# Kernel tuning notes

Hardware: AMD Instinct MI355X
Metric: run time of the kernel (lower is better)

## Reference

```python
import jax, jax.numpy as jnp
import numpy as np
from jax import lax

T, V, E = 8, 10000, 100000
C_IN, H, DS, C_OUT = 128, 256, 16, 64


def setup_inputs() -> dict:
    key = jax.random.key(0)
    ks = jax.random.split(key, 32)
    def nrm(k, shp, s=0.02):
        return jax.random.normal(k, shp, jnp.float32) * s
    inp = {}
    inp['xs'] = jax.random.normal(ks[0], (T, V, C_IN), jnp.float32)
    inp['edge_index'] = jax.random.randint(ks[1], (T, 2, E), 0, V, jnp.int64)
    # pre token mixer: depthwise conv1d over time, kernel 3, pad 1
    inp['w_pre'] = nrm(ks[2], (C_IN, 3), 0.3)
    inp['b_pre'] = jnp.zeros((C_IN,), jnp.float32)
    # per-layer params; layer 0 input C_IN, layer 1 input H
    for i, f in enumerate([C_IN, H]):
        o = 3 + i * 9
        inp[f'w_res{i}'] = nrm(ks[o + 0], (f, H))
        inp[f'b_res{i}'] = jnp.zeros((H,), jnp.float32)
        inp[f'w_self{i}'] = nrm(ks[o + 1], (f, H))
        inp[f'w_neigh{i}'] = nrm(ks[o + 2], (f, H))
        inp[f'b_sage{i}'] = jnp.zeros((H,), jnp.float32)
        inp[f'a_log{i}'] = nrm(ks[o + 3], (H, DS), 0.5)  # Lambda = exp(-exp(a_log)) in (0,1)
        inp[f'B{i}'] = nrm(ks[o + 4], (H, DS), 0.1)
        inp[f'w_mix{i}'] = nrm(ks[o + 5], (H * DS, H))
        inp[f'b_mix{i}'] = jnp.zeros((H,), jnp.float32)
    inp['w_out'] = nrm(ks[25], (H, C_OUT))
    inp['b_out'] = jnp.zeros((C_OUT,), jnp.float32)
    return inp


def _token_mix(xs, w, b):
    # xs: [T, V, C]; depthwise conv over time, kernel 3, zero pad 1
    xp = jnp.pad(xs, ((1, 1), (0, 0), (0, 0)))
    return xp[0:T] * w[:, 0] + xp[1:T + 1] * w[:, 1] + xp[2:T + 2] * w[:, 2] + b


def _sage(x, ei, w_self, w_neigh, b):
    # x: [V, C]; ei: [2, E]; mean aggregation of source features at target nodes
    src, dst = ei[0], ei[1]
    agg = jax.ops.segment_sum(x[src], dst, num_segments=V)          # [V, C]
    deg = jax.ops.segment_sum(jnp.ones((E,), x.dtype), dst, num_segments=V)
    mean = agg / jnp.maximum(deg, 1.0)[:, None]
    return x @ w_self + mean @ w_neigh + b


def _layer(xs, ei, w_res, b_res, w_self, w_neigh, b_sage, a_log, Bp, w_mix, b_mix):
    xsr = xs @ w_res + b_res                                        # [T, V, H]
    h = jax.vmap(_sage, in_axes=(0, 0, None, None, None))(xs, ei, w_self, w_neigh, b_sage)
    lam = jnp.exp(-jnp.exp(a_log))                                  # [H, DS]
    def step(state, x_t):
        state = lam * state + x_t[:, :, None] * Bp                  # [V, H, DS]
        y = jax.nn.relu(state.reshape(V, H * DS)) @ w_mix + b_mix   # [V, H]
        return state, y
    _, ys = lax.scan(step, jnp.zeros((V, H, DS), xs.dtype), h)
    return ys + xsr


def reference(xs, edge_index, w_pre, b_pre,
              w_res0, b_res0, w_self0, w_neigh0, b_sage0, a_log0, B0, w_mix0, b_mix0,
              w_res1, b_res1, w_self1, w_neigh1, b_sage1, a_log1, B1, w_mix1, b_mix1,
              w_out, b_out):
    xs = _token_mix(xs, w_pre, b_pre)
    xs = _layer(xs, edge_index, w_res0, b_res0, w_self0, w_neigh0, b_sage0, a_log0, B0, w_mix0, b_mix0)
    xs = _layer(xs, edge_index, w_res1, b_res1, w_self1, w_neigh1, b_sage1, a_log1, B1, w_mix1, b_mix1)
    return xs[-1] @ w_out + b_out
```

## Files before the change

### kernel.cpp

```cpp
#include <hip/hip_runtime.h>
#include <cstdint>
#include <cstddef>

#define T_DIM 8
#define V_DIM 10000
#define E_DIM 100000
#define M_ALL (T_DIM * V_DIM)

typedef __attribute__((ext_vector_type(8))) short short8;
typedef __attribute__((ext_vector_type(4))) float floatx4;

__device__ __forceinline__ unsigned int f2bf(float f) {
    union { float f; unsigned int u; } v; v.f = f;
    unsigned int u = v.u;
    u = u + 0x7FFFu + ((u >> 16) & 1u);
    return u >> 16;
}
__device__ __forceinline__ float bf2f(unsigned int s) {
    union { unsigned int u; float f; } v; v.u = s << 16;
    return v.f;
}
__device__ __forceinline__ short8 relu8(short8 x) {
    const short8 z = {0,0,0,0,0,0,0,0};
    return __builtin_elementwise_max(x, z);
}
union PK { uint4 u; short8 s; };

__global__ void pack_b_kernel(const float* __restrict__ w, unsigned short* __restrict__ out,
                              int K, int Nw, int NTN_tot, int nt_off, int kt_off) {
    int tid = blockIdx.x * blockDim.x + threadIdx.x;
    int total = (K >> 5) * (Nw >> 4) * 64;
    if (tid >= total) return;
    int lane = tid & 63;
    int f = tid >> 6;
    int ntn_w = Nw >> 4;
    int nt = f % ntn_w;
    int kt = f / ntn_w;
    int kbase = kt * 32 + ((lane >> 4) << 3);
    int n = nt * 16 + (lane & 15);
    unsigned int vals[8];
#pragma unroll
    for (int j = 0; j < 8; ++j)
        vals[j] = f2bf(w[(size_t)(kbase + j) * Nw + n]);
    uint4 pk;
    pk.x = vals[0] | (vals[1] << 16);
    pk.y = vals[2] | (vals[3] << 16);
    pk.z = vals[4] | (vals[5] << 16);
    pk.w = vals[6] | (vals[7] << 16);
    size_t fo = (size_t)(kt + kt_off) * NTN_tot + nt_off + nt;
    *(uint4*)(out + (fo * 64 + lane) * 8) = pk;
}

__global__ void token_mix_kernel(const float* __restrict__ xs, const float* __restrict__ w_pre,
                                 const float* __restrict__ b_pre, unsigned short* __restrict__ ob) {
    const int S = V_DIM * 128;
    int tid = blockIdx.x * blockDim.x + threadIdx.x;
    if (tid >= T_DIM * S / 4) return;
    int e = tid * 4;
    int t = e / S;
    int c = e & 127;
    floatx4 xm = {0.f,0.f,0.f,0.f}, xp = {0.f,0.f,0.f,0.f};
    floatx4 x0 = *(const floatx4*)(xs + e);
    if (t > 0)          xm = *(const floatx4*)(xs + e - S);
    if (t < T_DIM - 1)  xp = *(const floatx4*)(xs + e + S);
    uint2 p; unsigned int b[4];
#pragma unroll
    for (int j = 0; j < 4; ++j) {
        int cc = c + j;
        float r = xm[j]*w_pre[cc*3+0] + x0[j]*w_pre[cc*3+1] + xp[j]*w_pre[cc*3+2] + b_pre[cc];
        b[j] = f2bf(r);
    }
    p.x = b[0] | (b[1] << 16);
    p.y = b[2] | (b[3] << 16);
    *(uint2*)(ob + e) = p;
}

__global__ void lam_kernel(const float* __restrict__ a0, const float* __restrict__ a1,
                           float* __restrict__ lam0, float* __restrict__ lam1) {
    int i = blockIdx.x * blockDim.x + threadIdx.x;
    if (i >= 4096) return;
    lam0[i] = expf(-expf(a0[i]));
    lam1[i] = expf(-expf(a1[i]));
}

__global__ void bias_prep_kernel(const float* __restrict__ bs0, const float* __restrict__ bs1,
                                 const float* __restrict__ bm0, const float* __restrict__ br0,
                                 const float* __restrict__ bm1, const float* __restrict__ br1,
                                 float* __restrict__ bcat0, float* __restrict__ bcat1,
                                 float* __restrict__ bmt0, float* __restrict__ bmt1) {
    int i = blockIdx.x * blockDim.x + threadIdx.x;
    if (i < 512) {
        bcat0[i] = (i < 256) ? bs0[i] : 0.f;
        bcat1[i] = (i < 256) ? bs1[i] : 0.f;
    }
    if (i < 256) {
        bmt0[i] = bm0[i] + br0[i];
        bmt1[i] = bm1[i] + br1[i];
    }
}

__global__ void deg_kernel(const int* __restrict__ ei, int* __restrict__ deg_cnt) {
    int tid = blockIdx.x * blockDim.x + threadIdx.x;
    if (tid >= T_DIM * E_DIM) return;
    int t = tid / E_DIM;
    int e = tid - t * E_DIM;
    int dst = ei[(size_t)t * 2 * E_DIM + E_DIM + e];
    if ((unsigned)dst < V_DIM) atomicAdd(deg_cnt + t * V_DIM + dst, 1);
}

__global__ void invdeg_kernel(const int* __restrict__ deg_cnt, float* __restrict__ inv) {
    int tid = blockIdx.x * blockDim.x + threadIdx.x;
    if (tid >= T_DIM * V_DIM) return;
    inv[tid] = 1.0f / (float)max(deg_cnt[tid], 1);
}

__global__ __launch_bounds__(1024)
void scan_kernel(const int* __restrict__ deg_cnt, int* __restrict__ rowptr) {
    __shared__ int sums[1024];
    int t = blockIdx.x;
    const int* d = deg_cnt + t * V_DIM;
    int* rp = rowptr + t * (V_DIM + 1);
    int tid = threadIdx.x;
    int base = tid * 10;
    int loc[10]; int s = 0;
#pragma unroll
    for (int j = 0; j < 10; ++j) {
        int v = base + j;
        int x = (v < V_DIM) ? d[v] : 0;
        loc[j] = s; s += x;
    }
    sums[tid] = s;
    __syncthreads();
    for (int o = 1; o < 1024; o <<= 1) {
        int v = (tid >= o) ? sums[tid - o] : 0;
        __syncthreads();
        sums[tid] += v;
        __syncthreads();
    }
    int prev = (tid == 0) ? 0 : sums[tid - 1];
#pragma unroll
    for (int j = 0; j < 10; ++j) {
        int v = base + j;
        if (v < V_DIM) rp[v] = prev + loc[j];
    }
    if (tid == 1023) rp[V_DIM] = sums[1023];
}

__global__ void fill_kernel(const int* __restrict__ ei, const int* __restrict__ rowptr,
                            int* __restrict__ fill_cnt, int* __restrict__ srcs) {
    int tid = blockIdx.x * blockDim.x + threadIdx.x;
    if (tid >= T_DIM * E_DIM) return;
    int t = tid / E_DIM;
    int e = tid - t * E_DIM;
    const int* eit = ei + (size_t)t * 2 * E_DIM;
    int src = eit[e];
    int dst = eit[E_DIM + e];
    if ((unsigned)src >= V_DIM || (unsigned)dst >= V_DIM) return;
    int pos = rowptr[t * (V_DIM + 1) + dst] + atomicAdd(fill_cnt + t * V_DIM + dst, 1);
    srcs[(size_t)t * E_DIM + pos] = src;
}

__global__ void gather_pack_kernel(const unsigned short* __restrict__ xn, const int* __restrict__ srcs,
                                   const int* __restrict__ rowptr, const float* __restrict__ invdeg,
                                   const unsigned short* __restrict__ hb,
                                   unsigned short* __restrict__ hpack) {
    int gw = (blockIdx.x * blockDim.x + threadIdx.x) >> 6;
    int lane = threadIdx.x & 63;
    if (gw >= T_DIM * V_DIM) return;
    int t = gw / V_DIM;
    int v = gw - t * V_DIM;
    const int* rp = rowptr + t * (V_DIM + 1);
    int beg = rp[v], end = rp[v + 1];
    const int* st = srcs + (size_t)t * E_DIM;
    const unsigned short* xnt = xn + (size_t)t * V_DIM * 256;
    float a0 = 0.f, a1 = 0.f, a2 = 0.f, a3 = 0.f;
    for (int i = beg; i < end; ++i) {
        int s = st[i];
        uint2 p = *(const uint2*)(xnt + (size_t)s * 256 + lane * 4);
        a0 += bf2f(p.x & 0xffffu);
        a1 += bf2f(p.x >> 16);
        a2 += bf2f(p.y & 0xffffu);
        a3 += bf2f(p.y >> 16);
    }
    float inv = invdeg[t * V_DIM + v];
    uint2 h = *(const uint2*)(hb + ((size_t)t * V_DIM + v) * 256 + lane * 4);
    a0 = a0 * inv + bf2f(h.x & 0xffffu);
    a1 = a1 * inv + bf2f(h.x >> 16);
    a2 = a2 * inv + bf2f(h.y & 0xffffu);
    a3 = a3 * inv + bf2f(h.y >> 16);
    unsigned short* op = hpack + (size_t)v * 2048 + (size_t)(lane * 4) * 8 + t;
    op[0]  = (unsigned short)f2bf(a0);
    op[8]  = (unsigned short)f2bf(a1);
    op[16] = (unsigned short)f2bf(a2);
    op[24] = (unsigned short)f2bf(a3);
}

template<int KT>
__global__ __launch_bounds__(256, 4)
void gemm_cat2_kernel(const unsigned short* __restrict__ A, const unsigned short* __restrict__ Bp,
                      const float* __restrict__ bias, unsigned short* __restrict__ d_self,
                      unsigned short* __restrict__ d_xn, int M) {
    const int w = threadIdx.x >> 6, lane = threadIdx.x & 63;
    const int quad = lane >> 4, l16 = lane & 15;
    const int region = blockIdx.x;
    const int m0 = blockIdx.y * 64;
    constexpr int K = KT * 32;
    floatx4 acc[4][4];
#pragma unroll
    for (int a = 0; a < 4; ++a)
#pragma unroll
        for (int b = 0; b < 4; ++b) acc[a][b] = (floatx4){0.f,0.f,0.f,0.f};
    const unsigned short* arow[4];
#pragma unroll
    for (int mi = 0; mi < 4; ++mi) {
        int r = m0 + mi * 16 + l16;
        if (r > M - 1) r = M - 1;
        arow[mi] = A + (size_t)r * K + quad * 8;
    }
    const unsigned short* bptr = Bp + ((size_t)(region * 16 + w * 4) * 64 + lane) * 8;
#pragma unroll
    for (int kt = 0; kt < KT; ++kt) {
        short8 bfr[4];
#pragma unroll
        for (int i = 0; i < 4; ++i) bfr[i] = *(const short8*)(bptr + i * 512);
        short8 af[4];
#pragma unroll
        for (int mi = 0; mi < 4; ++mi) af[mi] = *(const short8*)(arow[mi]);
#pragma unroll
        for (int mi = 0; mi < 4; ++mi)
#pragma unroll
            for (int i = 0; i < 4; ++i)
                acc[mi][i] = __builtin_amdgcn_mfma_f32_16x16x32_bf16(af[mi], bfr[i], acc[mi][i], 0, 0, 0);
        bptr += 32 * 512;
#pragma unroll
        for (int mi = 0; mi < 4; ++mi) arow[mi] += 32;
    }
#pragma unroll
    for (int mi = 0; mi < 4; ++mi) {
        int rbase = m0 + mi * 16 + quad * 4;
#pragma unroll
        for (int i = 0; i < 4; ++i) {
            int lcol = w * 64 + i * 16 + l16;
            float b = bias[region * 256 + lcol];
#pragma unroll
            for (int rr = 0; rr < 4; ++rr) {
                int row = rbase + rr;
                if (row < M) {
                    float v = acc[mi][i][rr] + b;
                    size_t off = (size_t)row * 256 + lcol;
                    if (region == 0) d_self[off] = (unsigned short)f2bf(v);
                    else             d_xn[off]  = (unsigned short)f2bf(v);
                }
            }
        }
    }
}

template<int NT, int KRT>
__global__ __launch_bounds__(256, 2)
void gemm_mix_rec2_kernel(const unsigned short* __restrict__ hp,
                          const unsigned short* __restrict__ Bp,
                          const unsigned short* __restrict__ Ares,
                          const float* __restrict__ lam,
                          const float* __restrict__ Bv,
                          const float* __restrict__ bias,
                          unsigned short* __restrict__ out) {
    constexpr int KR = KRT * 32;
    __shared__ __align__(16) unsigned short Afrag[2][4 * NT * 64 * 8];
    const int tid = threadIdx.x;
    const int w = tid >> 6, lane = tid & 63;
    const int quad = lane >> 4, l16 = lane & 15;
    const int m0 = blockIdx.x * 16;
    const int prow = tid & 15;
    const int oct  = tid >> 4;
    const int kt_w = oct >> 2, qo = oct & 3;
    const int vr = m0 + prow;

    floatx4 acc[NT][4];
#pragma unroll
    for (int t = 0; t < NT; ++t)
#pragma unroll
        for (int i = 0; i < 4; ++i) acc[t][i] = (floatx4){0.f,0.f,0.f,0.f};

    const unsigned short* bptr = Bp + ((size_t)(w * 4) * 64 + lane) * 8;

    auto compute = [&](int ph, int buf) {
        const int kg = ph * 128 + kt_w * 32 + qo * 8;
        const int ch = kg >> 4;
        PK h8; h8.u = *(const uint4*)(hp + (size_t)vr * 2048 + (size_t)ch * 8);
        floatx4 l0 = *(const floatx4*)(lam + kg);
        floatx4 l1 = *(const floatx4*)(lam + kg + 4);
        floatx4 b0 = *(const floatx4*)(Bv + kg);
        floatx4 b1 = *(const floatx4*)(Bv + kg + 4);
        float s0=0.f,s1=0.f,s2=0.f,s3=0.f,s4=0.f,s5=0.f,s6=0.f,s7=0.f;
        unsigned short* ap = Afrag[buf] + ((size_t)(kt_w * NT) * 64 + qo * 16 + prow) * 8;
#pragma unroll
        for (int t = 0; t < 8; ++t) {
            float hv = bf2f((unsigned int)(unsigned short)h8.s[t]);
            s0 = l0[0]*s0 + hv*b0[0];
            s1 = l0[1]*s1 + hv*b0[1];
            s2 = l0[2]*s2 + hv*b0[2];
            s3 = l0[3]*s3 + hv*b0[3];
            s4 = l1[0]*s4 + hv*b1[0];
            s5 = l1[1]*s5 + hv*b1[1];
            s6 = l1[2]*s6 + hv*b1[2];
            s7 = l1[3]*s7 + hv*b1[3];
            if (NT == 8 || t == 7) {
                PK cv;
                cv.u.x = f2bf(s0) | (f2bf(s1) << 16);
                cv.u.y = f2bf(s2) | (f2bf(s3) << 16);
                cv.u.z = f2bf(s4) | (f2bf(s5) << 16);
                cv.u.w = f2bf(s6) | (f2bf(s7) << 16);
                PK st; st.s = relu8(cv.s);
                *(uint4*)(ap + (size_t)((NT == 8) ? t : 0) * 512) = st.u;
            }
        }
    };
    auto consume = [&](int buf) {
#pragma unroll
        for (int kt = 0; kt < 4; ++kt) {
            short8 bfr[4];
#pragma unroll
            for (int i = 0; i < 4; ++i) bfr[i] = *(const short8*)(bptr + i * 512);
#pragma unroll
            for (int t = 0; t < NT; ++t) {
                short8 af = *(const short8*)(Afrag[buf] + (size_t)((kt * NT + t) * 64 + lane) * 8);
#pragma unroll
                for (int i = 0; i < 4; ++i)
                    acc[t][i] = __builtin_amdgcn_mfma_f32_16x16x32_bf16(af, bfr[i], acc[t][i], 0, 0, 0);
            }
            bptr += 16 * 512;
        }
    };

    compute(0, 0);
    __syncthreads();
    for (int ph = 0; ph < 32; ++ph) {
        if (ph < 31) compute(ph + 1, (ph + 1) & 1);
        consume(ph & 1);
        __syncthreads();
    }

#pragma unroll
    for (int ktr = 0; ktr < KRT; ++ktr) {
        short8 bfr[4];
#pragma unroll
        for (int i = 0; i < 4; ++i) bfr[i] = *(const short8*)(bptr + i * 512);
#pragma unroll
        for (int t = 0; t < NT; ++t) {
            const unsigned short* ar = Ares + ((size_t)t * V_DIM + (size_t)(m0 + l16)) * KR + ktr * 32 + quad * 8;
            short8 af = *(const short8*)ar;
#pragma unroll
            for (int i = 0; i < 4; ++i)
                acc[t][i] = __builtin_amdgcn_mfma_f32_16x16x32_bf16(af, bfr[i], acc[t][i], 0, 0, 0);
        }
        bptr += 16 * 512;
    }
#pragma unroll
    for (int t = 0; t < NT; ++t) {
#pragma unroll
        for (int i = 0; i < 4; ++i) {
            int col = w * 64 + i * 16 + l16;
            float b = bias[col];
#pragma unroll
            for (int rr = 0; rr < 4; ++rr) {
                int row = m0 + quad * 4 + rr;
                out[((size_t)t * V_DIM + row) * 256 + col] = (unsigned short)f2bf(acc[t][i][rr] + b);
            }
        }
    }
}

template<int NT, int NTN_TOT, bool RELU>
__global__ __launch_bounds__(512)
void gemm16_kernel(const unsigned short* __restrict__ A, const unsigned short* __restrict__ Bp,
                   const float* __restrict__ bias, float* __restrict__ outF, int M, int K) {
    const int w = threadIdx.x >> 6, lane = threadIdx.x & 63;
    const int quad = lane >> 4, l16 = lane & 15;
    const int rowgrp = w >> 2, nchunk = w & 3;
    const int m0 = blockIdx.x * 32 + rowgrp * 16;
    const int ntb = nchunk * NT;
    constexpr int Ntot = NTN_TOT * 16;
    floatx4 acc[NT];
#pragma unroll
    for (int i = 0; i < NT; ++i) acc[i] = (floatx4){0.f,0.f,0.f,0.f};
    int r = m0 + l16; if (r > M - 1) r = M - 1;
    const unsigned short* arow = A + (size_t)r * K + quad * 8;
    const int ksteps = K >> 5;
    for (int kt = 0; kt < ksteps; ++kt) {
        short8 af = *(const short8*)(arow + kt * 32);
        if (RELU) af = relu8(af);
#pragma unroll
        for (int i = 0; i < NT; ++i) {
            short8 bf = *(const short8*)(Bp + ((size_t)(kt * NTN_TOT + ntb + i) * 64 + lane) * 8);
            acc[i] = __builtin_amdgcn_mfma_f32_16x16x32_bf16(af, bf, acc[i], 0, 0, 0);
        }
    }
    const int rbase = m0 + quad * 4;
#pragma unroll
    for (int i = 0; i < NT; ++i) {
        int col = (ntb + i) * 16 + l16;
        float b = bias[col];
#pragma unroll
        for (int rr = 0; rr < 4; ++rr) {
            int row = rbase + rr;
            if (row < M)
                outF[(size_t)row * Ntot + col] = acc[i][rr] + b;
        }
    }
}

extern "C" void kernel_launch(void* const* d_in, const int* in_sizes, int n_in,
                              void* d_out, int out_size, void* d_ws, size_t ws_size,
                              hipStream_t stream) {
    const float* xs      = (const float*)d_in[0];
    const int*   ei      = (const int*)d_in[1];
    const float* w_pre   = (const float*)d_in[2];
    const float* b_pre   = (const float*)d_in[3];
    const float* w_res0  = (const float*)d_in[4];
    const float* b_res0  = (const float*)d_in[5];
    const float* w_self0 = (const float*)d_in[6];
    const float* w_neigh0= (const float*)d_in[7];
    const float* b_sage0 = (const float*)d_in[8];
    const float* a_log0  = (const float*)d_in[9];
    const float* B0      = (const float*)d_in[10];
    const float* w_mix0  = (const float*)d_in[11];
    const float* b_mix0  = (const float*)d_in[12];
    const float* w_res1  = (const float*)d_in[13];
    const float* b_res1  = (const float*)d_in[14];
    const float* w_self1 = (const float*)d_in[15];
    const float* w_neigh1= (const float*)d_in[16];
    const float* b_sage1 = (const float*)d_in[17];
    const float* a_log1  = (const float*)d_in[18];
    const float* B1      = (const float*)d_in[19];
    const float* w_mix1  = (const float*)d_in[20];
    const float* b_mix1  = (const float*)d_in[21];
    const float* w_out   = (const float*)d_in[22];
    const float* b_out   = (const float*)d_in[23];

    char* wsB = (char*)d_ws;
    size_t off = 0;
    auto alloc = [&](size_t bytes) {
        char* p = wsB + off;
        off += (bytes + 255) & ~(size_t)255;
        return p;
    };
    unsigned short* x0b   = (unsigned short*)alloc((size_t)M_ALL * 128 * 2);
    unsigned short* hA    = (unsigned short*)alloc((size_t)M_ALL * 256 * 2);
    unsigned short* hB    = (unsigned short*)alloc((size_t)M_ALL * 256 * 2);
    unsigned short* hpack = (unsigned short*)alloc((size_t)V_DIM * 2048 * 2);
    unsigned short* x1b   = (unsigned short*)alloc((size_t)M_ALL * 256 * 2);
    unsigned short* out1_b= (unsigned short*)alloc((size_t)V_DIM * 256 * 2);
    int*            deg_cnt = (int*)alloc((size_t)T_DIM * V_DIM * 4);
    float*          invdeg  = (float*)alloc((size_t)T_DIM * V_DIM * 4);
    int*            rowptr  = (int*)alloc((size_t)T_DIM * (V_DIM + 1) * 4);
    int*            fill_cnt= (int*)alloc((size_t)T_DIM * V_DIM * 4);
    int*            srcs    = (int*)alloc((size_t)T_DIM * E_DIM * 4);
    float*          lam0  = (float*)alloc(4096 * 4);
    float*          lam1  = (float*)alloc(4096 * 4);
    float*          bcat0 = (float*)alloc(512 * 4);
    float*          bcat1 = (float*)alloc(512 * 4);
    float*          bmt0  = (float*)alloc(256 * 4);
    float*          bmt1  = (float*)alloc(256 * 4);
    unsigned short* wcat0p= (unsigned short*)alloc((size_t)128 * 512 * 2);
    unsigned short* wcat1p= (unsigned short*)alloc((size_t)256 * 512 * 2);
    unsigned short* wmix0p= (unsigned short*)alloc((size_t)(4096 + 128) * 256 * 2);
    unsigned short* wmix1p= (unsigned short*)alloc((size_t)(4096 + 256) * 256 * 2);
    unsigned short* woutp = (unsigned short*)alloc((size_t)256 * 64 * 2);
    if (off > ws_size) return;

    auto cdiv = [](int a, int b) { return (a + b - 1) / b; };
    const int gMall = cdiv(M_ALL, 64);
    const int gGat  = cdiv(M_ALL * 64, 256);

    lam_kernel<<<16, 256, 0, stream>>>(a_log0, a_log1, lam0, lam1);
    bias_prep_kernel<<<2, 256, 0, stream>>>(b_sage0, b_sage1, b_mix0, b_res0, b_mix1, b_res1,
                                            bcat0, bcat1, bmt0, bmt1);
    pack_b_kernel<<<cdiv(4*16*64, 256), 256, 0, stream>>>(w_self0,  wcat0p, 128, 256, 32, 0, 0);
    pack_b_kernel<<<cdiv(4*16*64, 256), 256, 0, stream>>>(w_neigh0, wcat0p, 128, 256, 32, 16, 0);
    pack_b_kernel<<<cdiv(8*16*64, 256), 256, 0, stream>>>(w_self1,  wcat1p, 256, 256, 32, 0, 0);
    pack_b_kernel<<<cdiv(8*16*64, 256), 256, 0, stream>>>(w_neigh1, wcat1p, 256, 256, 32, 16, 0);
    pack_b_kernel<<<cdiv(128*16*64, 256), 256, 0, stream>>>(w_mix0, wmix0p, 4096, 256, 16, 0, 0);
    pack_b_kernel<<<cdiv(4*16*64, 256),   256, 0, stream>>>(w_res0, wmix0p, 128,  256, 16, 0, 128);
    pack_b_kernel<<<cdiv(128*16*64, 256), 256, 0, stream>>>(w_mix1, wmix1p, 4096, 256, 16, 0, 0);
    pack_b_kernel<<<cdiv(8*16*64, 256),   256, 0, stream>>>(w_res1, wmix1p, 256,  256, 16, 0, 128);
    pack_b_kernel<<<cdiv(8*4*64, 256), 256, 0, stream>>>(w_out, woutp, 256, 64, 4, 0, 0);

    token_mix_kernel<<<cdiv(T_DIM*V_DIM*128/4, 256), 256, 0, stream>>>(xs, w_pre, b_pre, x0b);
    hipMemsetAsync(deg_cnt, 0, (size_t)T_DIM * V_DIM * 4, stream);
    hipMemsetAsync(fill_cnt, 0, (size_t)T_DIM * V_DIM * 4, stream);
    deg_kernel<<<cdiv(T_DIM*E_DIM, 256), 256, 0, stream>>>(ei, deg_cnt);
    scan_kernel<<<T_DIM, 1024, 0, stream>>>(deg_cnt, rowptr);
    invdeg_kernel<<<cdiv(T_DIM*V_DIM, 256), 256, 0, stream>>>(deg_cnt, invdeg);
    fill_kernel<<<cdiv(T_DIM*E_DIM, 256), 256, 0, stream>>>(ei, rowptr, fill_cnt, srcs);

    gemm_cat2_kernel<4><<<dim3(2, gMall), 256, 0, stream>>>(x0b, wcat0p, bcat0, hA, hB, M_ALL);
    gather_pack_kernel<<<gGat, 256, 0, stream>>>(hB, srcs, rowptr, invdeg, hA, hpack);
    gemm_mix_rec2_kernel<8, 4><<<V_DIM / 16, 256, 0, stream>>>(
        hpack, wmix0p, x0b, lam0, B0, bmt0, x1b);

    gemm_cat2_kernel<8><<<dim3(2, gMall), 256, 0, stream>>>(x1b, wcat1p, bcat1, hA, hB, M_ALL);
    gather_pack_kernel<<<gGat, 256, 0, stream>>>(hB, srcs, rowptr, invdeg, hA, hpack);
    gemm_mix_rec2_kernel<1, 8><<<V_DIM / 16, 256, 0, stream>>>(
        hpack, wmix1p, x1b + (size_t)(T_DIM - 1) * V_DIM * 256, lam1, B1, bmt1, out1_b);

    gemm16_kernel<1, 4, false><<<cdiv(V_DIM,32), 512, 0, stream>>>(
        out1_b, woutp, b_out, (float*)d_out, V_DIM, 256);
}
```

Baseline: 982.9 us.

## Halve mix-kernel phase size, split state work per thread, use hardware bf16 pack

Measured after the change: 997.1 us. Within noise of the previous version (+1.4%).

```diff
diff --git a/kernel.cpp b/kernel.cpp
--- a/kernel.cpp
+++ b/kernel.cpp
@@ -8,6 +8,7 @@
 #define M_ALL (T_DIM * V_DIM)
 
 typedef __attribute__((ext_vector_type(8))) short short8;
+typedef __attribute__((ext_vector_type(4))) short sx4;
 typedef __attribute__((ext_vector_type(4))) float floatx4;
 
 __device__ __forceinline__ unsigned int f2bf(float f) {
@@ -24,7 +25,17 @@
     const short8 z = {0,0,0,0,0,0,0,0};
     return __builtin_elementwise_max(x, z);
 }
+__device__ __forceinline__ sx4 relu4(sx4 x) {
+    const sx4 z = {0,0,0,0};
+    return __builtin_elementwise_max(x, z);
+}
+__device__ __forceinline__ unsigned int cvtpk_bf16(float lo, float hi) {
+    unsigned int r;
+    asm("v_cvt_pk_bf16_f32 %0, %1, %2" : "=v"(r) : "v"(lo), "v"(hi));
+    return r;
+}
 union PK { uint4 u; short8 s; };
+union PK2 { uint2 u; sx4 s; };
 
 __global__ void pack_b_kernel(const float* __restrict__ w, unsigned short* __restrict__ out,
                               int K, int Nw, int NTN_tot, int nt_off, int kt_off) {
@@ -258,7 +269,7 @@
 
 template<int NT, int KRT>
 __global__ __launch_bounds__(256, 2)
-void gemm_mix_rec2_kernel(const unsigned short* __restrict__ hp,
+void gemm_mix_rec3_kernel(const unsigned short* __restrict__ hp,
                           const unsigned short* __restrict__ Bp,
                           const unsigned short* __restrict__ Ares,
                           const float* __restrict__ lam,
@@ -266,14 +277,17 @@
                           const float* __restrict__ bias,
                           unsigned short* __restrict__ out) {
     constexpr int KR = KRT * 32;
-    __shared__ __align__(16) unsigned short Afrag[2][4 * NT * 64 * 8];
+    __shared__ __align__(16) unsigned short Afrag[2][2 * NT * 64 * 8];
     const int tid = threadIdx.x;
     const int w = tid >> 6, lane = tid & 63;
     const int quad = lane >> 4, l16 = lane & 15;
     const int m0 = blockIdx.x * 16;
     const int prow = tid & 15;
-    const int oct  = tid >> 4;
-    const int kt_w = oct >> 2, qo = oct & 3;
+    const int g    = tid >> 4;
+    const int kt_w = g >> 3;
+    const int sub  = g & 7;
+    const int qo   = sub >> 1;
+    const int hf   = sub & 1;
     const int vr = m0 + prow;
 
     floatx4 acc[NT][4];
@@ -285,43 +299,36 @@
     const unsigned short* bptr = Bp + ((size_t)(w * 4) * 64 + lane) * 8;
 
     auto compute = [&](int ph, int buf) {
-        const int kg = ph * 128 + kt_w * 32 + qo * 8;
+        const int kg = ph * 64 + kt_w * 32 + qo * 8 + hf * 4;
         const int ch = kg >> 4;
         PK h8; h8.u = *(const uint4*)(hp + (size_t)vr * 2048 + (size_t)ch * 8);
-        floatx4 l0 = *(const floatx4*)(lam + kg);
-        floatx4 l1 = *(const floatx4*)(lam + kg + 4);
-        floatx4 b0 = *(const floatx4*)(Bv + kg);
-        floatx4 b1 = *(const floatx4*)(Bv + kg + 4);
-        float s0=0.f,s1=0.f,s2=0.f,s3=0.f,s4=0.f,s5=0.f,s6=0.f,s7=0.f;
-        unsigned short* ap = Afrag[buf] + ((size_t)(kt_w * NT) * 64 + qo * 16 + prow) * 8;
+        floatx4 l = *(const floatx4*)(lam + kg);
+        floatx4 b = *(const floatx4*)(Bv + kg);
+        float s0 = 0.f, s1 = 0.f, s2 = 0.f, s3 = 0.f;
+        unsigned short* ap = Afrag[buf] + ((size_t)(kt_w * NT) * 64 + qo * 16 + prow) * 8 + hf * 4;
 #pragma unroll
         for (int t = 0; t < 8; ++t) {
             float hv = bf2f((unsigned int)(unsigned short)h8.s[t]);
-            s0 = l0[0]*s0 + hv*b0[0];
-            s1 = l0[1]*s1 + hv*b0[1];
-            s2 = l0[2]*s2 + hv*b0[2];
-            s3 = l0[3]*s3 + hv*b0[3];
-            s4 = l1[0]*s4 + hv*b1[0];
-            s5 = l1[1]*s5 + hv*b1[1];
-            s6 = l1[2]*s6 + hv*b1[2];
-            s7 = l1[3]*s7 + hv*b1[3];
+            s0 = l[0]*s0 + hv*b[0];
+            s1 = l[1]*s1 + hv*b[1];
+            s2 = l[2]*s2 + hv*b[2];
+            s3 = l[3]*s3 + hv*b[3];
             if (NT == 8 || t == 7) {
-                PK cv;
-                cv.u.x = f2bf(s0) | (f2bf(s1) << 16);
-                cv.u.y = f2bf(s2) | (f2bf(s3) << 16);
-                cv.u.z = f2bf(s4) | (f2bf(s5) << 16);
-                cv.u.w = f2bf(s6) | (f2bf(s7) << 16);
-                PK st; st.s = relu8(cv.s);
-                *(uint4*)(ap + (size_t)((NT == 8) ? t : 0) * 512) = st.u;
+                PK2 cv;
+                cv.u.x = cvtpk_bf16(s0, s1);
+                cv.u.y = cvtpk_bf16(s2, s3);
+                PK2 st; st.s = relu4(cv.s);
+                *(uint2*)(ap + (size_t)((NT == 8) ? t : 0) * 512) = st.u;
             }
         }
     };
     auto consume = [&](int buf) {
 #pragma unroll
-        for (int kt = 0; kt < 4; ++kt) {
+        for (int kt = 0; kt < 2; ++kt) {
             short8 bfr[4];
 #pragma unroll
             for (int i = 0; i < 4; ++i) bfr[i] = *(const short8*)(bptr + i * 512);
+            __builtin_amdgcn_s_setprio(1);
 #pragma unroll
             for (int t = 0; t < NT; ++t) {
                 short8 af = *(const short8*)(Afrag[buf] + (size_t)((kt * NT + t) * 64 + lane) * 8);
@@ -329,14 +336,15 @@
                 for (int i = 0; i < 4; ++i)
                     acc[t][i] = __builtin_amdgcn_mfma_f32_16x16x32_bf16(af, bfr[i], acc[t][i], 0, 0, 0);
             }
+            __builtin_amdgcn_s_setprio(0);
             bptr += 16 * 512;
         }
     };
 
     compute(0, 0);
     __syncthreads();
-    for (int ph = 0; ph < 32; ++ph) {
-        if (ph < 31) compute(ph + 1, (ph + 1) & 1);
+    for (int ph = 0; ph < 64; ++ph) {
+        if (ph < 63) compute(ph + 1, (ph + 1) & 1);
         consume(ph & 1);
         __syncthreads();
     }
@@ -496,12 +504,12 @@
 
     gemm_cat2_kernel<4><<<dim3(2, gMall), 256, 0, stream>>>(x0b, wcat0p, bcat0, hA, hB, M_ALL);
     gather_pack_kernel<<<gGat, 256, 0, stream>>>(hB, srcs, rowptr, invdeg, hA, hpack);
-    gemm_mix_rec2_kernel<8, 4><<<V_DIM / 16, 256, 0, stream>>>(
+    gemm_mix_rec3_kernel<8, 4><<<V_DIM / 16, 256, 0, stream>>>(
         hpack, wmix0p, x0b, lam0, B0, bmt0, x1b);
 
     gemm_cat2_kernel<8><<<dim3(2, gMall), 256, 0, stream>>>(x1b, wcat1p, bcat1, hA, hB, M_ALL);
     gather_pack_kernel<<<gGat, 256, 0, stream>>>(hB, srcs, rowptr, invdeg, hA, hpack);
-    gemm_mix_rec2_kernel<1, 8><<<V_DIM / 16, 256, 0, stream>>>(
+    gemm_mix_rec3_kernel<1, 8><<<V_DIM / 16, 256, 0, stream>>>(
         hpack, wmix1p, x1b + (size_t)(T_DIM - 1) * V_DIM * 256, lam1, B1, bmt1, out1_b);
 
     gemm16_kernel<1, 4, false><<<cdiv(V_DIM,32), 512, 0, stream>>>(
```

## Split mix-recurrence GEMM over time chunks and use hardware bf16 pack

Applied to the files above, without the earlier changes.

Measured after the change: 926.2 us. -5.8%, faster.

```diff
diff --git a/kernel.cpp b/kernel.cpp
--- a/kernel.cpp
+++ b/kernel.cpp
@@ -23,6 +23,11 @@
 __device__ __forceinline__ short8 relu8(short8 x) {
     const short8 z = {0,0,0,0,0,0,0,0};
     return __builtin_elementwise_max(x, z);
+}
+__device__ __forceinline__ unsigned int cvtpk_bf16(float lo, float hi) {
+    unsigned int r;
+    asm("v_cvt_pk_bf16_f32 %0, %1, %2" : "=v"(r) : "v"(lo), "v"(hi));
+    return r;
 }
 union PK { uint4 u; short8 s; };
 
@@ -256,29 +261,31 @@
     }
 }
 
-template<int NT, int KRT>
-__global__ __launch_bounds__(256, 2)
-void gemm_mix_rec2_kernel(const unsigned short* __restrict__ hp,
+template<int NTC, int KRT>
+__global__ __launch_bounds__(256, 3)
+void gemm_mix_rec4_kernel(const unsigned short* __restrict__ hp,
                           const unsigned short* __restrict__ Bp,
                           const unsigned short* __restrict__ Ares,
                           const float* __restrict__ lam,
                           const float* __restrict__ Bv,
                           const float* __restrict__ bias,
-                          unsigned short* __restrict__ out) {
+                          unsigned short* __restrict__ out,
+                          int T0base, int OB) {
     constexpr int KR = KRT * 32;
-    __shared__ __align__(16) unsigned short Afrag[2][4 * NT * 64 * 8];
+    __shared__ __align__(16) unsigned short Afrag[2][4 * NTC * 64 * 8];
     const int tid = threadIdx.x;
     const int w = tid >> 6, lane = tid & 63;
     const int quad = lane >> 4, l16 = lane & 15;
-    const int m0 = blockIdx.x * 16;
+    const int T0 = T0base + blockIdx.x * NTC;
+    const int m0 = blockIdx.y * 16;
     const int prow = tid & 15;
     const int oct  = tid >> 4;
     const int kt_w = oct >> 2, qo = oct & 3;
     const int vr = m0 + prow;
 
-    floatx4 acc[NT][4];
-#pragma unroll
-    for (int t = 0; t < NT; ++t)
+    floatx4 acc[NTC][4];
+#pragma unroll
+    for (int t = 0; t < NTC; ++t)
 #pragma unroll
         for (int i = 0; i < 4; ++i) acc[t][i] = (floatx4){0.f,0.f,0.f,0.f};
 
@@ -293,7 +300,7 @@
         floatx4 b0 = *(const floatx4*)(Bv + kg);
         floatx4 b1 = *(const floatx4*)(Bv + kg + 4);
         float s0=0.f,s1=0.f,s2=0.f,s3=0.f,s4=0.f,s5=0.f,s6=0.f,s7=0.f;
-        unsigned short* ap = Afrag[buf] + ((size_t)(kt_w * NT) * 64 + qo * 16 + prow) * 8;
+        unsigned short* ap = Afrag[buf] + ((size_t)(kt_w * NTC) * 64 + qo * 16 + prow) * 8;
 #pragma unroll
         for (int t = 0; t < 8; ++t) {
             float hv = bf2f((unsigned int)(unsigned short)h8.s[t]);
@@ -305,14 +312,14 @@
             s5 = l1[1]*s5 + hv*b1[1];
             s6 = l1[2]*s6 + hv*b1[2];
             s7 = l1[3]*s7 + hv*b1[3];
-            if (NT == 8 || t == 7) {
+            if ((unsigned)(t - T0) < (unsigned)NTC) {
                 PK cv;
-                cv.u.x = f2bf(s0) | (f2bf(s1) << 16);
-                cv.u.y = f2bf(s2) | (f2bf(s3) << 16);
-                cv.u.z = f2bf(s4) | (f2bf(s5) << 16);
-                cv.u.w = f2bf(s6) | (f2bf(s7) << 16);
+                cv.u.x = cvtpk_bf16(s0, s1);
+                cv.u.y = cvtpk_bf16(s2, s3);
+                cv.u.z = cvtpk_bf16(s4, s5);
+                cv.u.w = cvtpk_bf16(s6, s7);
                 PK st; st.s = relu8(cv.s);
-                *(uint4*)(ap + (size_t)((NT == 8) ? t : 0) * 512) = st.u;
+                *(uint4*)(ap + (size_t)(t - T0) * 512) = st.u;
             }
         }
     };
@@ -322,13 +329,15 @@
             short8 bfr[4];
 #pragma unroll
             for (int i = 0; i < 4; ++i) bfr[i] = *(const short8*)(bptr + i * 512);
-#pragma unroll
-            for (int t = 0; t < NT; ++t) {
-                short8 af = *(const short8*)(Afrag[buf] + (size_t)((kt * NT + t) * 64 + lane) * 8);
+            __builtin_amdgcn_s_setprio(1);
+#pragma unroll
+            for (int ts = 0; ts < NTC; ++ts) {
+                short8 af = *(const short8*)(Afrag[buf] + (size_t)((kt * NTC + ts) * 64 + lane) * 8);
 #pragma unroll
                 for (int i = 0; i < 4; ++i)
-                    acc[t][i] = __builtin_amdgcn_mfma_f32_16x16x32_bf16(af, bfr[i], acc[t][i], 0, 0, 0);
+                    acc[ts][i] = __builtin_amdgcn_mfma_f32_16x16x32_bf16(af, bfr[i], acc[ts][i], 0, 0, 0);
             }
+            __builtin_amdgcn_s_setprio(0);
             bptr += 16 * 512;
         }
     };
@@ -347,17 +356,17 @@
 #pragma unroll
         for (int i = 0; i < 4; ++i) bfr[i] = *(const short8*)(bptr + i * 512);
 #pragma unroll
-        for (int t = 0; t < NT; ++t) {
-            const unsigned short* ar = Ares + ((size_t)t * V_DIM + (size_t)(m0 + l16)) * KR + ktr * 32 + quad * 8;
+        for (int ts = 0; ts < NTC; ++ts) {
+            const unsigned short* ar = Ares + ((size_t)(T0 + ts) * V_DIM + (size_t)(m0 + l16)) * KR + ktr * 32 + quad * 8;
             short8 af = *(const short8*)ar;
 #pragma unroll
             for (int i = 0; i < 4; ++i)
-                acc[t][i] = __builtin_amdgcn_mfma_f32_16x16x32_bf16(af, bfr[i], acc[t][i], 0, 0, 0);
+                acc[ts][i] = __builtin_amdgcn_mfma_f32_16x16x32_bf16(af, bfr[i], acc[ts][i], 0, 0, 0);
         }
         bptr += 16 * 512;
     }
 #pragma unroll
-    for (int t = 0; t < NT; ++t) {
+    for (int ts = 0; ts < NTC; ++ts) {
 #pragma unroll
         for (int i = 0; i < 4; ++i) {
             int col = w * 64 + i * 16 + l16;
@@ -365,7 +374,7 @@
 #pragma unroll
             for (int rr = 0; rr < 4; ++rr) {
                 int row = m0 + quad * 4 + rr;
-                out[((size_t)t * V_DIM + row) * 256 + col] = (unsigned short)f2bf(acc[t][i][rr] + b);
+                out[((size_t)(T0 + ts - OB) * V_DIM + row) * 256 + col] = (unsigned short)f2bf(acc[ts][i][rr] + b);
             }
         }
     }
@@ -496,13 +505,13 @@
 
     gemm_cat2_kernel<4><<<dim3(2, gMall), 256, 0, stream>>>(x0b, wcat0p, bcat0, hA, hB, M_ALL);
     gather_pack_kernel<<<gGat, 256, 0, stream>>>(hB, srcs, rowptr, invdeg, hA, hpack);
-    gemm_mix_rec2_kernel<8, 4><<<V_DIM / 16, 256, 0, stream>>>(
-        hpack, wmix0p, x0b, lam0, B0, bmt0, x1b);
+    gemm_mix_rec4_kernel<4, 4><<<dim3(2, V_DIM / 16), 256, 0, stream>>>(
+        hpack, wmix0p, x0b, lam0, B0, bmt0, x1b, 0, 0);
 
     gemm_cat2_kernel<8><<<dim3(2, gMall), 256, 0, stream>>>(x1b, wcat1p, bcat1, hA, hB, M_ALL);
     gather_pack_kernel<<<gGat, 256, 0, stream>>>(hB, srcs, rowptr, invdeg, hA, hpack);
-    gemm_mix_rec2_kernel<1, 8><<<V_DIM / 16, 256, 0, stream>>>(
-        hpack, wmix1p, x1b + (size_t)(T_DIM - 1) * V_DIM * 256, lam1, B1, bmt1, out1_b);
+    gemm_mix_rec4_kernel<1, 8><<<dim3(1, V_DIM / 16), 256, 0, stream>>>(
+        hpack, wmix1p, x1b, lam1, B1, bmt1, out1_b, 7, 7);
 
     gemm16_kernel<1, 4, false><<<cdiv(V_DIM,32), 512, 0, stream>>>(
         out1_b, woutp, b_out, (float*)d_out, V_DIM, 256);
```
